# Performance work log

Hardware: AMD Instinct MI355X
Metric: run time of the kernel (lower is better)

Reference implementation:

```python
import jax, jax.numpy as jnp
import numpy as np
from jax import lax

B, N, T, HOR, HID = 512, 128, 128, 32, 512


def _uni(k, shape, s):
    return jax.random.uniform(k, shape, jnp.float32, -s, s)


def setup_inputs() -> dict:
    key = jax.random.key(0)
    ks = jax.random.split(key, 24)
    s = 1.0 / np.sqrt(HID)
    inp = {"window": jax.random.normal(ks[0], (B * N, T), jnp.float32)}
    # encoder LSTM (2 layers, torch gate order i,f,g,o)
    inp["Wih0"] = _uni(ks[1], (4 * HID, N), s); inp["Whh0"] = _uni(ks[2], (4 * HID, HID), s)
    inp["bih0"] = _uni(ks[3], (4 * HID,), s);   inp["bhh0"] = _uni(ks[4], (4 * HID,), s)
    inp["Wih1"] = _uni(ks[5], (4 * HID, HID), s); inp["Whh1"] = _uni(ks[6], (4 * HID, HID), s)
    inp["bih1"] = _uni(ks[7], (4 * HID,), s);     inp["bhh1"] = _uni(ks[8], (4 * HID,), s)
    # decoder cells
    inp["Wc1i"] = _uni(ks[9], (4 * HID, N), s);   inp["Wc1h"] = _uni(ks[10], (4 * HID, HID), s)
    inp["bc1i"] = _uni(ks[11], (4 * HID,), s);    inp["bc1h"] = _uni(ks[12], (4 * HID,), s)
    inp["Wc2i"] = _uni(ks[13], (4 * HID, HID), s); inp["Wc2h"] = _uni(ks[14], (4 * HID, HID), s)
    inp["bc2i"] = _uni(ks[15], (4 * HID,), s);     inp["bc2h"] = _uni(ks[16], (4 * HID,), s)
    # output projection
    inp["Wp"] = _uni(ks[17], (N, HID), s); inp["bp"] = _uni(ks[18], (N,), s)
    # deterministic inverted-dropout masks
    keep_e = 0.75  # nn.LSTM inter-layer dropout p=0.25
    keep_d = 0.8   # F.dropout p=0.2 in decode loop
    inp["enc_mask"] = (jax.random.uniform(ks[19], (T, B, HID)) < keep_e).astype(jnp.float32) / keep_e
    inp["dec_h_mask"] = (jax.random.uniform(ks[20], (HOR - 1, B, HID)) < keep_d).astype(jnp.float32) / keep_d
    inp["dec_c_mask"] = (jax.random.uniform(ks[21], (HOR - 1, B, HID)) < keep_d).astype(jnp.float32) / keep_d
    return inp


def _cell(x, h, c, Wih, Whh, bih, bhh):
    g = x @ Wih.T + h @ Whh.T + (bih + bhh)
    i, f, gg, o = jnp.split(g, 4, axis=-1)
    c = jax.nn.sigmoid(f) * c + jax.nn.sigmoid(i) * jnp.tanh(gg)
    h = jax.nn.sigmoid(o) * jnp.tanh(c)
    return h, c


def _run_layer(xs, Wih, Whh, bih, bhh):
    # xs: [T, B, D] -> outputs [T, B, HID], final (h, c)
    h0 = jnp.zeros((xs.shape[1], HID), xs.dtype)
    def step(carry, x):
        h, c = carry
        h, c = _cell(x, h, c, Wih, Whh, bih, bhh)
        return (h, c), h
    (h, c), hs = lax.scan(step, (h0, h0), xs)
    return hs, h, c


def reference(window, Wih0, Whh0, bih0, bhh0, Wih1, Whh1, bih1, bhh1,
              Wc1i, Wc1h, bc1i, bc1h, Wc2i, Wc2h, bc2i, bc2h, Wp, bp,
              enc_mask, dec_h_mask, dec_c_mask):
    x = window.reshape(B, T, N).transpose(1, 0, 2)  # [T, B, N]
    hs0, h1, c1 = _run_layer(x, Wih0, Whh0, bih0, bhh0)
    hs0 = hs0 * enc_mask  # inter-layer dropout (training mode)
    _, h2, c2 = _run_layer(hs0, Wih1, Whh1, bih1, bhh1)

    def dec_step(carry, masks):
        h1, c1, h2, c2 = carry
        mh, mc = masks
        pred = h2 @ Wp.T + bp                       # [B, N]
        h1, c1 = _cell(pred, h1, c1, Wc1i, Wc1h, bc1i, bc1h)
        h1 = h1 * mh
        c1 = c1 * mc
        h2, c2 = _cell(h1, h2, c2, Wc2i, Wc2h, bc2i, bc2h)
        return (h1, c1, h2, c2), pred

    (h1, c1, h2, c2), preds = lax.scan(dec_step, (h1, c1, h2, c2), (dec_h_mask, dec_c_mask))
    final = h2 @ Wp.T + bp                          # [B, N]
    allp = jnp.concatenate([preds, final[None]], axis=0)  # [HOR, B, N]
    # torch: each pred.view(-1,1), cat dim=1 -> [B*N, HOR]
    return allp.transpose(1, 2, 0).reshape(B * N, HOR)
```

## Files before the change

### kernel.cpp

```cpp
#include <hip/hip_runtime.h>
#include <math.h>

#define HID 512
#define BAT 512
#define NIN 128
#define TST 128
#define HOR 32
#define SBZ ((size_t)BAT * HID)
#define SL 262144
#define SLB 524288

using bf16x8 = __attribute__((ext_vector_type(8))) __bf16;
using f32x4  = __attribute__((ext_vector_type(4))) float;

__device__ __forceinline__ float sigf(float x) { return 1.0f / (1.0f + __expf(-x)); }
__device__ __forceinline__ float tanhfast(float x) { return 1.0f - 2.0f / (__expf(2.0f * x) + 1.0f); }

__device__ __forceinline__ short f2bf(float x) {
    union { float f; unsigned u; } v; v.f = x;
    unsigned r = (v.u + 0x7FFFu + ((v.u >> 16) & 1u)) >> 16;
    return (short)r;
}
__device__ __forceinline__ float bf2f(short s) {
    union { unsigned u; float f; } v; v.u = ((unsigned)(unsigned short)s) << 16;
    return v.f;
}
__device__ __forceinline__ bf16x8 asbf(f32x4 v) {
    union { f32x4 f; bf16x8 b; } u; u.f = v; return u.b;
}

__device__ __forceinline__ void gbar3(unsigned* bar, int bid, unsigned ep) {
    __syncthreads();
    if (threadIdx.x == 0) {
        unsigned* leaf = bar + ((unsigned)bid >> 3) * 32;
        unsigned* root = bar + 1024;
        unsigned* flag = bar + 1056;
        unsigned old = __hip_atomic_fetch_add(leaf, 1u, __ATOMIC_RELAXED, __HIP_MEMORY_SCOPE_AGENT);
        if (old == 8u * ep - 1u) {
            unsigned ro = __hip_atomic_fetch_add(root, 1u, __ATOMIC_RELAXED, __HIP_MEMORY_SCOPE_AGENT);
            if (ro == 32u * ep - 1u)
                __hip_atomic_store(flag, ep, __ATOMIC_RELAXED, __HIP_MEMORY_SCOPE_AGENT);
        }
        int spin = 0;
        while (__hip_atomic_load(flag, __ATOMIC_RELAXED, __HIP_MEMORY_SCOPE_AGENT) < ep) {
            __builtin_amdgcn_s_sleep(1);
            if (((++spin) & 63) == 0)
                __hip_atomic_fetch_add(flag, 0u, __ATOMIC_RELAXED, __HIP_MEMORY_SCOPE_AGENT);
        }
    }
    __syncthreads();
}


__global__ __launch_bounds__(256) void prep_w(const float* __restrict__ Wih,
                                              const float* __restrict__ Whh,
                                              short* __restrict__ W2, int Kx, int Kp) {
    size_t i = (size_t)blockIdx.x * 256 + threadIdx.x;
    if (i >= (size_t)2048 * Kp) return;
    int np = (int)(i / Kp), kp = (int)(i % Kp);
    int u = np >> 2, gate = np & 3;
    int on = gate * HID + u;
    float w = (kp < Kx) ? Wih[(size_t)on * Kx + kp] : Whh[(size_t)on * HID + (kp - Kx)];
    W2[i] = f2bf(w);
}

__global__ __launch_bounds__(256) void prep_x(const float* __restrict__ window,
                                              short* __restrict__ X2t) {
    size_t i = (size_t)blockIdx.x * 256 + threadIdx.x;
    if (i >= (size_t)TST * BAT * NIN) return;
    int n = (int)(i & 127);
    int b = (int)((i >> 7) & 511);
    int t = (int)(i >> 16);
    float x = window[(size_t)b * (TST * NIN) + (size_t)t * NIN + n];
    int rg = b >> 4;
    int l = (b & 15) + (((n >> 3) & 3) << 4);
    int e = n & 7;
    size_t base = (size_t)t * 65536 + ((size_t)(rg * 4 + (n >> 5)) << 9) + l * 8 + e;
    X2t[base] = f2bf(x);
}

__global__ __launch_bounds__(256) void prep_fuse(const float* __restrict__ Wc1i,
                                                 const float* __restrict__ Wp,
                                                 float* __restrict__ Wfuse) {
    size_t i = (size_t)blockIdx.x * 256 + threadIdx.x;
    if (i >= (size_t)2048 * 512) return;
    int on = (int)(i >> 9), k = (int)(i & 511);
    float s = 0.f;
    for (int n = 0; n < NIN; ++n) s += Wc1i[(size_t)on * NIN + n] * Wp[(size_t)n * HID + k];
    Wfuse[i] = s;
}

__global__ __launch_bounds__(256) void prep_badd(const float* __restrict__ Wc1i,
                                                 const float* __restrict__ bp,
                                                 float* __restrict__ badd) {
    int on = blockIdx.x * 256 + threadIdx.x;
    if (on >= 2048) return;
    float s = 0.f;
    for (int n = 0; n < NIN; ++n) s += Wc1i[(size_t)on * NIN + n] * bp[n];
    badd[on] = s;
}

__global__ __launch_bounds__(256) void prep_bias(const float* __restrict__ bih,
                                                 const float* __restrict__ bhh,
                                                 const float* __restrict__ badd,
                                                 float* __restrict__ bout) {
    int np = blockIdx.x * 256 + threadIdx.x;
    if (np >= 2048) return;
    int on = (np & 3) * HID + (np >> 2);
    float v = bih[on] + bhh[on];
    if (badd) v += badd[on];
    bout[np] = v;
}

__global__ __launch_bounds__(256) void prep_wp(const float* __restrict__ Wp,
                                               short* __restrict__ W2p) {
    int i = blockIdx.x * 256 + threadIdx.x;
    if (i >= 128 * 512) return;
    W2p[i] = f2bf(Wp[i]);
}


__device__ __forceinline__ void gl16sc(f32x4& q, const char* p) {
    asm volatile("global_load_dwordx4 %0, %1, off sc0 sc1" : "=v"(q) : "v"(p));
}

__device__ __forceinline__ void load_wres32(char* lds, const short* Wg, int K) {
    const int tid = threadIdx.x;
    const int r = tid >> 4;
    const int cnt = K >> 7;
    const int jb = (tid & 15) * cnt;
    for (int q = 0; q < cnt; ++q) {
        int j = jb + q;
        bf16x8 v = *(const bf16x8*)(Wg + (size_t)r * K + j * 8);
        *(bf16x8*)(lds + j * 512 + r * 16) = v;
    }
}

__device__ __forceinline__ void load_wres64(char* lds, const short* Wg, int K) {
    const int r = threadIdx.x >> 2, jg = threadIdx.x & 3;
    for (int q = 0; q < (K >> 5); ++q) {
        int j = jg + (q << 2);
        bf16x8 v = *(const bf16x8*)(Wg + (size_t)r * K + j * 8);
        *(bf16x8*)(lds + (size_t)j * 1024 + r * 16) = v;
    }
}

__device__ __forceinline__ void pre_mask_asm(const float* msk, int mrow, int u0, float o[4]) {
    const int lane = threadIdx.x & 63;
    const float* p = msk + (size_t)(mrow + ((lane >> 3) << 2)) * HID + u0 + (lane & 7);
#pragma unroll
    for (int r = 0; r < 4; ++r)
        asm volatile("global_load_dword %0, %1, off" : "=v"(o[r]) : "v"(p + (size_t)r * HID));
}

template<int C0, int C1>
__device__ __forceinline__ void gemm64(
    const char* wres, const short* a0t, const short* a1t,
    int mb, f32x4 acc[2][4])
{
    constexpr int NKC = C0 + C1;
    constexpr int D = 16;
    const int lane = threadIdx.x & 63;
    const int arow = lane & 15, akg = lane >> 4;
    const size_t lb = (size_t)lane << 4;
    const char* base0 = (const char*)a0t;
    const char* base1 = (const char*)a1t;
    auto cptr = [&](int kc, int fh) -> const char* {
        return (kc < C0)
            ? base0 + (((size_t)(mb * 2 + fh) * C0 + kc) << 10) + lb
            : base1 + (((size_t)(mb * 2 + fh) * C1 + (kc - C0)) << 10) + lb;
    };
    f32x4 q0[D], q1[D];
#pragma unroll
    for (int i = 0; i < D; ++i) {
        gl16sc(q0[i], cptr(i, 0));
        gl16sc(q1[i], cptr(i, 1));
    }
#pragma unroll
    for (int kc = 0; kc < NKC; ++kc) {
        const int sl = kc % D;
        asm volatile("s_waitcnt vmcnt(%2)"
                     : "+v"(q0[sl]), "+v"(q1[sl])
                     : "i"((2 * ((NKC - kc) < D ? (NKC - kc) : D)) - 2));
        const bf16x8 fa0 = asbf(q0[sl]);
        const bf16x8 fa1 = asbf(q1[sl]);
        if (kc + D < NKC) {
            gl16sc(q0[sl], cptr(kc + D, 0));
            gl16sc(q1[sl], cptr(kc + D, 1));
        }
        const char* wrow = wres + (size_t)((kc << 2) + akg) * 1024;
        bf16x8 fb[4];
#pragma unroll
        for (int nj = 0; nj < 4; ++nj)
            fb[nj] = *(const bf16x8*)(wrow + ((nj * 16 + arow) << 4));
#pragma unroll
        for (int nj = 0; nj < 4; ++nj) {
            acc[0][nj] = __builtin_amdgcn_mfma_f32_16x16x32_bf16(fa0, fb[nj], acc[0][nj], 0, 0, 0);
            acc[1][nj] = __builtin_amdgcn_mfma_f32_16x16x32_bf16(fa1, fb[nj], acc[1][nj], 0, 0, 0);
        }
    }
    asm volatile("s_waitcnt vmcnt(0)");
}

__device__ __forceinline__ void cell_epi64(
    char* scrw, f32x4 acc[2][4], float creg[2][4], int mb, int np0,
    const float* bias_p, const float* mh, const float* mc, const float* ma,
    short* h_out, short* h_aux)
{
    const int lane = threadIdx.x & 63;
#pragma unroll
    for (int p = 0; p < 2; ++p) {
        const int np0p = np0 + (p << 5);
#pragma unroll
        for (int mi = 0; mi < 2; ++mi)
#pragma unroll
            for (int nj = 0; nj < 2; ++nj) {
                const int row = mi * 16 + ((lane >> 4) << 2);
                const int col = nj * 16 + (lane & 15);
#pragma unroll
                for (int r = 0; r < 4; ++r)
                    *(float*)(scrw + (row + r) * 128 + (col << 2)) = acc[mi][p * 2 + nj][r];
            }
        asm volatile("s_waitcnt lgkmcnt(0)" ::: "memory");
        const int ul = lane & 7, g = lane >> 3;
        f32x4 gv[4];
#pragma unroll
        for (int r = 0; r < 4; ++r)
            gv[r] = *(const f32x4*)(scrw + ((g << 2) + r) * 128 + (ul << 4));
        asm volatile("s_waitcnt lgkmcnt(0)" ::: "memory");
        const float4 bs = *(const float4*)(bias_p + np0p + (ul << 2));
#pragma unroll
        for (int r = 0; r < 4; ++r) {
            const int m = (g << 2) + r;
            const int fh = m >> 4, r16 = m & 15;
            const float gi = gv[r][0] + bs.x, gf = gv[r][1] + bs.y;
            const float gg = gv[r][2] + bs.z, go = gv[r][3] + bs.w;
            const float cn = sigf(gf) * creg[p][r] + sigf(gi) * tanhfast(gg);
            const float h  = sigf(go) * tanhfast(cn);
            creg[p][r] = mc ? cn * mc[p * 4 + r] : cn;
            const float hm = mh ? h * mh[p * 4 + r] : h;
            const int idx2 = (r16 << 3) + ul;
            *(short*)(scrw + fh * 256 + idx2 * 2) = f2bf(hm);
            if (h_aux)
                *(short*)(scrw + 512 + fh * 256 + idx2 * 2) = f2bf(h * ma[p * 4 + r]);
        }
        const int u0p = np0p >> 2;
        const int c_hi = u0p >> 5, gsub = (u0p >> 3) & 3;
        unsigned vmain[2], vaux[2];
#pragma unroll
        for (int s = 0; s < 2; ++s)
            vmain[s] = *(const unsigned*)(scrw + s * 256 + (lane << 2));
        if (h_aux)
#pragma unroll
            for (int s = 0; s < 2; ++s)
                vaux[s] = *(const unsigned*)(scrw + 512 + s * 256 + (lane << 2));
        asm volatile("s_waitcnt lgkmcnt(0)" ::: "memory");
#pragma unroll
        for (int s = 0; s < 2; ++s) {
            const unsigned* dst = (const unsigned*)(h_out
                + ((size_t)((mb * 2 + s) * 16 + c_hi) << 9) + (gsub << 7)) + lane;
            asm volatile("global_store_dword %0, %1, off sc0 sc1" :: "v"(dst), "v"(vmain[s]));
        }
        if (h_aux)
#pragma unroll
            for (int s = 0; s < 2; ++s) {
                const unsigned* dst = (const unsigned*)(h_aux
                    + ((size_t)((mb * 2 + s) * 16 + c_hi) << 9) + (gsub << 7)) + lane;
                asm volatile("global_store_dword %0, %1, off sc0 sc1" :: "v"(dst), "v"(vaux[s]));
            }
    }
}


__global__ void __launch_bounds__(256, 1) persist_kernel(
    const short* __restrict__ X2t,
    const short* __restrict__ W0, const short* __restrict__ W1,
    const short* __restrict__ Wd1, const short* __restrict__ Wd2,
    short* hA0, short* hA1, short* hd0, short* hd1, short* hB0, short* hB1,
    short* hBall0, short* hBallR,
    const float* __restrict__ bias0, const float* __restrict__ bias1,
    const float* __restrict__ biasd1, const float* __restrict__ biasd2,
    const float* __restrict__ enc_mask, const float* __restrict__ dec_h_mask,
    const float* __restrict__ dec_c_mask, unsigned* bar)
{
    extern __shared__ __align__(16) char lds[];
    const int bid = blockIdx.x;
    const int xcd = bid & 7;
    const int half = xcd >> 2;
    const int m0 = (xcd & 3) * 128;
    const int ntile = bid >> 3;
    const int np0 = ntile * 64;
    const int u0 = np0 >> 2;
    const int w = threadIdx.x >> 6;
    const int mb = (m0 >> 5) + w;
    const int mrow = m0 + (w << 5);
    char* scrw = lds + 131072 + (w << 12);
    float creg[2][4] = {{0.f,0.f,0.f,0.f},{0.f,0.f,0.f,0.f}};

    auto hA_rd = [&](int t) -> const short* { return (t & 1) ? hA1 : hA0; };
    auto hA_wr = [&](int t) -> short* { return (t & 1) ? hA0 : hA1; };
    auto hd_at = [&](int t) -> short* { return (t & 1) ? hd1 : hd0; };
    auto hB_rd = [&](int t) -> const short* { return (t & 1) ? hB1 : hB0; };
    auto hB_wr = [&](int t) -> short* { return (t & 1) ? hB0 : hB1; };
    auto decA_at = [&](int i) -> short* { return (i & 1) ? hA1 : hA0; };
    auto hball = [&](int i) -> short* { return (i == 0) ? hBall0 : hBallR + (size_t)(i - 1) * SL; };

    load_wres64(lds, (half ? W1 : W0) + (size_t)np0 * (half ? 1024 : 640), half ? 1024 : 640);
    __syncthreads();
    unsigned ep = 0;
    for (int tt = 0; tt <= TST; ++tt) {
        if (half == 0) {
            if (tt < TST) {
                const int t = tt;
                float ma[8];
                pre_mask_asm(enc_mask + (size_t)t * SBZ, mrow, u0, ma);
                pre_mask_asm(enc_mask + (size_t)t * SBZ, mrow, u0 + 8, ma + 4);
                f32x4 acc[2][4];
#pragma unroll
                for (int a = 0; a < 2; ++a)
#pragma unroll
                    for (int b2 = 0; b2 < 4; ++b2) acc[a][b2] = (f32x4){0.f, 0.f, 0.f, 0.f};
                gemm64<4, 16>(lds, X2t + (size_t)t * 65536, hA_rd(t), mb, acc);
                cell_epi64(scrw, acc, creg, mb, np0, bias0, nullptr, nullptr, ma,
                           hA_wr(t), hd_at(t));
            }
        } else {
            if (tt >= 1) {
                const int t = tt - 1;
                f32x4 acc[2][4];
#pragma unroll
                for (int a = 0; a < 2; ++a)
#pragma unroll
                    for (int b2 = 0; b2 < 4; ++b2) acc[a][b2] = (f32x4){0.f, 0.f, 0.f, 0.f};
                gemm64<16, 16>(lds, hd_at(t), hB_rd(t), mb, acc);
                short* outp = (t == TST - 1) ? hBall0 : hB_wr(t);
                cell_epi64(scrw, acc, creg, mb, np0, bias1, nullptr, nullptr, nullptr,
                           outp, nullptr);
            }
        }
        gbar3(bar, bid, ++ep);
    }

    load_wres64(lds, (half ? Wd2 : Wd1) + (size_t)np0 * 1024, 1024);
    __syncthreads();
    for (int s = 0; s < HOR - 1; ++s) {
        if (half == 0) {
            float mh[8], mc[8];
            pre_mask_asm(dec_h_mask + (size_t)s * SBZ, mrow, u0, mh);
            pre_mask_asm(dec_h_mask + (size_t)s * SBZ, mrow, u0 + 8, mh + 4);
            pre_mask_asm(dec_c_mask + (size_t)s * SBZ, mrow, u0, mc);
            pre_mask_asm(dec_c_mask + (size_t)s * SBZ, mrow, u0 + 8, mc + 4);
            f32x4 acc[2][4];
#pragma unroll
            for (int a = 0; a < 2; ++a)
#pragma unroll
                for (int b2 = 0; b2 < 4; ++b2) acc[a][b2] = (f32x4){0.f, 0.f, 0.f, 0.f};
            gemm64<16, 16>(lds, hball(s), decA_at(s), mb, acc);
            cell_epi64(scrw, acc, creg, mb, np0, biasd1, mh, mc, nullptr,
                       decA_at(s + 1), nullptr);
        }
        gbar3(bar, bid, ++ep);
        if (half == 1) {
            f32x4 acc[2][4];
#pragma unroll
            for (int a = 0; a < 2; ++a)
#pragma unroll
                for (int b2 = 0; b2 < 4; ++b2) acc[a][b2] = (f32x4){0.f, 0.f, 0.f, 0.f};
            gemm64<16, 16>(lds, decA_at(s + 1), hball(s), mb, acc);
            cell_epi64(scrw, acc, creg, mb, np0, biasd2, nullptr, nullptr, nullptr,
                       hball(s + 1), nullptr);
        }
        gbar3(bar, bid, ++ep);
    }
}


template<int C0, int C1>
__device__ __forceinline__ void gemm_pipeP(
    const char* wres, const short* a0t, const short* a1t,
    int mb, f32x4 acc[2][2])
{
    constexpr int NKC = C0 + C1;
    constexpr int D = 16;
    const int lane = threadIdx.x & 63;
    const int arow = lane & 15, akg = lane >> 4;
    const size_t lb = (size_t)lane << 4;
    const char* base0 = (const char*)a0t;
    const char* base1 = (const char*)a1t;
    auto cptr = [&](int kc, int fh) -> const char* {
        return (kc < C0)
            ? base0 + (((size_t)(mb * 2 + fh) * C0 + kc) << 10) + lb
            : base1 + (((size_t)(mb * 2 + fh) * C1 + (kc - C0)) << 10) + lb;
    };
    f32x4 q0[D], q1[D];
#pragma unroll
    for (int i = 0; i < D; ++i) {
        gl16sc(q0[i], cptr(i, 0));
        gl16sc(q1[i], cptr(i, 1));
    }
#pragma unroll
    for (int kc = 0; kc < NKC; ++kc) {
        const int sl = kc % D;
        asm volatile("s_waitcnt vmcnt(%2)"
                     : "+v"(q0[sl]), "+v"(q1[sl])
                     : "i"((2 * ((NKC - kc) < D ? (NKC - kc) : D)) - 2));
        const bf16x8 fa0 = asbf(q0[sl]);
        const bf16x8 fa1 = asbf(q1[sl]);
        if (kc + D < NKC) {
            gl16sc(q0[sl], cptr(kc + D, 0));
            gl16sc(q1[sl], cptr(kc + D, 1));
        }
        const char* wrow = wres + (size_t)(((kc << 2) + akg) << 9);
        const bf16x8 fb0 = *(const bf16x8*)(wrow + (arow << 4));
        const bf16x8 fb1 = *(const bf16x8*)(wrow + ((16 + arow) << 4));
        acc[0][0] = __builtin_amdgcn_mfma_f32_16x16x32_bf16(fa0, fb0, acc[0][0], 0, 0, 0);
        acc[0][1] = __builtin_amdgcn_mfma_f32_16x16x32_bf16(fa0, fb1, acc[0][1], 0, 0, 0);
        acc[1][0] = __builtin_amdgcn_mfma_f32_16x16x32_bf16(fa1, fb0, acc[1][0], 0, 0, 0);
        acc[1][1] = __builtin_amdgcn_mfma_f32_16x16x32_bf16(fa1, fb1, acc[1][1], 0, 0, 0);
    }
    asm volatile("s_waitcnt vmcnt(0)");
}

__global__ void __launch_bounds__(512, 2) proj_kernel(
    const short* hBall0, const short* hBallR, const short* __restrict__ W2p,
    const float* __restrict__ bp, float* __restrict__ pred_all)
{
    extern __shared__ __align__(16) char lds[];
    const int bid = blockIdx.x;
    const int s = bid >> 3, q = bid & 7;
    const int bh = q >> 2, n0p = (q & 3) * 32;
    load_wres32(lds, W2p + (size_t)n0p * 512, 512);
    const int w = threadIdx.x >> 6, lane = threadIdx.x & 63;
    char* scrw = lds + 32768 + w * 4608;
    const int mb = bh * 8 + w;
    const short* A = (s == 0) ? hBall0 : hBallR + (size_t)(s - 1) * SL;
    __syncthreads();
    f32x4 acc[2][2];
#pragma unroll
    for (int a = 0; a < 2; ++a)
#pragma unroll
        for (int b2 = 0; b2 < 2; ++b2) acc[a][b2] = (f32x4){0.f, 0.f, 0.f, 0.f};
    gemm_pipeP<16, 0>(lds, A, A, mb, acc);
#pragma unroll
    for (int mi = 0; mi < 2; ++mi)
#pragma unroll
        for (int ni = 0; ni < 2; ++ni) {
            const int row = mi * 16 + ((lane >> 4) << 2);
            const int col = ni * 16 + (lane & 15);
#pragma unroll
            for (int r = 0; r < 4; ++r)
                *(float*)(scrw + (row + r) * 144 + (col << 2)) = acc[mi][ni][r];
        }
    asm volatile("s_waitcnt lgkmcnt(0)" ::: "memory");
    const int rr = lane >> 1, hf = lane & 1;
    float* dst = pred_all + (size_t)s * (BAT * NIN)
               + (size_t)(bh * 256 + w * 32 + rr) * NIN + n0p + hf * 16;
#pragma unroll
    for (int t4 = 0; t4 < 4; ++t4) {
        f32x4 v = *(const f32x4*)(scrw + rr * 144 + hf * 64 + t4 * 16);
        const float4 b4 = *(const float4*)(bp + n0p + hf * 16 + t4 * 4);
        v[0] += b4.x; v[1] += b4.y; v[2] += b4.z; v[3] += b4.w;
        *(f32x4*)(dst + t4 * 4) = v;
    }
}

__global__ __launch_bounds__(256) void transpose_out(const float* __restrict__ pred_all,
                                                     float* __restrict__ out) {
    __shared__ float tl[32][65];
    const int base = blockIdx.x * 64;
    const int tid = threadIdx.x;
    for (int i = tid; i < 32 * 64; i += 256) {
        int s = i >> 6, f = i & 63;
        tl[s][f] = pred_all[(size_t)s * (BAT * NIN) + base + f];
    }
    __syncthreads();
    for (int i = tid; i < 64 * 32; i += 256) {
        int f = i >> 5, s = i & 31;
        out[(size_t)(base + f) * HOR + s] = tl[s][f];
    }
}


extern "C" void kernel_launch(void* const* d_in, const int* in_sizes, int n_in,
                              void* d_out, int out_size, void* d_ws, size_t ws_size,
                              hipStream_t stream) {
    (void)in_sizes; (void)n_in; (void)out_size; (void)ws_size;
    const float* window = (const float*)d_in[0];
    const float* Wih0 = (const float*)d_in[1];
    const float* Whh0 = (const float*)d_in[2];
    const float* bih0 = (const float*)d_in[3];
    const float* bhh0 = (const float*)d_in[4];
    const float* Wih1 = (const float*)d_in[5];
    const float* Whh1 = (const float*)d_in[6];
    const float* bih1 = (const float*)d_in[7];
    const float* bhh1 = (const float*)d_in[8];
    const float* Wc1i = (const float*)d_in[9];
    const float* Wc1h = (const float*)d_in[10];
    const float* bc1i = (const float*)d_in[11];
    const float* bc1h = (const float*)d_in[12];
    const float* Wc2i = (const float*)d_in[13];
    const float* Wc2h = (const float*)d_in[14];
    const float* bc2i = (const float*)d_in[15];
    const float* bc2h = (const float*)d_in[16];
    const float* Wp   = (const float*)d_in[17];
    const float* bp   = (const float*)d_in[18];
    const float* enc_mask   = (const float*)d_in[19];
    const float* dec_h_mask = (const float*)d_in[20];
    const float* dec_c_mask = (const float*)d_in[21];
    float* out = (float*)d_out;

    char* base = (char*)d_ws;
    size_t off = 0;
    auto take = [&](size_t bytes) -> char* {
        off = (off + 255) & ~(size_t)255;
        char* r = base + off; off += bytes; return r;
    };
    short* W2e0 = (short*)take((size_t)2048 * 640 * 2);
    short* W2e1 = (short*)take((size_t)2048 * 1024 * 2);
    short* W2d1 = (short*)take((size_t)2048 * 1024 * 2);
    short* W2d2 = (short*)take((size_t)2048 * 1024 * 2);
    short* W2p  = (short*)take((size_t)128 * 512 * 2);
    float* Wfuse = (float*)take((size_t)2048 * 512 * 4);
    float* badd  = (float*)take((size_t)2048 * 4);
    float* bias0 = (float*)take((size_t)2048 * 4);
    float* bias1 = (float*)take((size_t)2048 * 4);
    float* biasd1 = (float*)take((size_t)2048 * 4);
    float* biasd2 = (float*)take((size_t)2048 * 4);
    short* hBall0 = (short*)take(SLB);
    float* pred_all = (float*)take((size_t)HOR * BAT * NIN * 4);
    unsigned* bars = (unsigned*)take(16384);
    short* X2t = (short*)take((size_t)TST * 65536 * 2);
    short* hA0 = (short*)take(SLB);
    short* hA1 = (short*)take(SLB);
    short* hd0 = (short*)take(SLB);
    short* hd1 = (short*)take(SLB);
    short* hB0 = (short*)take(SLB);
    short* hB1 = (short*)take(SLB);
    short* hBallR = X2t;

    prep_fuse<<<(2048 * 512 + 255) / 256, 256, 0, stream>>>(Wc1i, Wp, Wfuse);
    prep_badd<<<8, 256, 0, stream>>>(Wc1i, bp, badd);
    prep_wp<<<(128 * 512 + 255) / 256, 256, 0, stream>>>(Wp, W2p);
    prep_w<<<(2048 * 640 + 255) / 256, 256, 0, stream>>>(Wih0, Whh0, W2e0, NIN, 640);
    prep_w<<<(2048 * 1024 + 255) / 256, 256, 0, stream>>>(Wih1, Whh1, W2e1, HID, 1024);
    prep_w<<<(2048 * 1024 + 255) / 256, 256, 0, stream>>>(Wfuse, Wc1h, W2d1, HID, 1024);
    prep_w<<<(2048 * 1024 + 255) / 256, 256, 0, stream>>>(Wc2i, Wc2h, W2d2, HID, 1024);
    prep_bias<<<8, 256, 0, stream>>>(bih0, bhh0, nullptr, bias0);
    prep_bias<<<8, 256, 0, stream>>>(bih1, bhh1, nullptr, bias1);
    prep_bias<<<8, 256, 0, stream>>>(bc1i, bc1h, badd, biasd1);
    prep_bias<<<8, 256, 0, stream>>>(bc2i, bc2h, nullptr, biasd2);
    prep_x<<<(int)(((size_t)TST * BAT * NIN + 255) / 256), 256, 0, stream>>>(window, X2t);
    hipMemsetAsync(hA0, 0, SLB, stream);
    hipMemsetAsync(hB0, 0, SLB, stream);
    hipMemsetAsync(bars, 0, 16384, stream);

    hipFuncSetAttribute((const void*)&persist_kernel,
                        hipFuncAttributeMaxDynamicSharedMemorySize, 163840);
    persist_kernel<<<256, 256, 147456, stream>>>(
        X2t, W2e0, W2e1, W2d1, W2d2,
        hA0, hA1, hd0, hd1, hB0, hB1,
        hBall0, hBallR,
        bias0, bias1, biasd1, biasd2,
        enc_mask, dec_h_mask, dec_c_mask, bars);

    hipFuncSetAttribute((const void*)&proj_kernel,
                        hipFuncAttributeMaxDynamicSharedMemorySize, 69632);
    proj_kernel<<<256, 512, 69632, stream>>>(hBall0, hBallR, W2p, bp, pred_all);

    transpose_out<<<(BAT * NIN) / 64, 256, 0, stream>>>(pred_all, out);
}
```

Baseline: 1.788 ms.

## Replace grid-wide barriers with per-batch-tile partial barriers and relax cache bypass

Each group of 64 blocks that shares a batch tile (mtile) now synchronises only with itself through a separate hierarchical barrier, instead of all 256 blocks using one grid barrier per step. A single grid barrier remains at the encoder/decoder boundary. Loads of read-only data (the X input slice, and activations in the projection kernel) drop the sc0/sc1 cache-bypass bits so they can hit in cache. The intent is lower barrier latency and cheaper loads, relying on the fact that each M tile's recurrence depends only on its own batch rows.

Measured after the change: 1.736 ms. 1.03x faster.

```diff
diff --git a/kernel.cpp b/kernel.cpp
--- a/kernel.cpp
+++ b/kernel.cpp
@@ -27,6 +27,28 @@
 }
 __device__ __forceinline__ bf16x8 asbf(f32x4 v) {
     union { f32x4 f; bf16x8 b; } u; u.f = v; return u.b;
+}
+
+__device__ __forceinline__ void pbar(unsigned* b, int sub, unsigned ep) {
+    __syncthreads();
+    if (threadIdx.x == 0) {
+        unsigned* leaf = b + (sub >> 3) * 32;
+        unsigned* root = b + 512;
+        unsigned* flag = b + 544;
+        unsigned old = __hip_atomic_fetch_add(leaf, 1u, __ATOMIC_RELAXED, __HIP_MEMORY_SCOPE_AGENT);
+        if (old == 8u * ep - 1u) {
+            unsigned ro = __hip_atomic_fetch_add(root, 1u, __ATOMIC_RELAXED, __HIP_MEMORY_SCOPE_AGENT);
+            if (ro == 8u * ep - 1u)
+                __hip_atomic_store(flag, ep, __ATOMIC_RELAXED, __HIP_MEMORY_SCOPE_AGENT);
+        }
+        int spin = 0;
+        while (__hip_atomic_load(flag, __ATOMIC_RELAXED, __HIP_MEMORY_SCOPE_AGENT) < ep) {
+            __builtin_amdgcn_s_sleep(1);
+            if (((++spin) & 63) == 0)
+                __hip_atomic_fetch_add(flag, 0u, __ATOMIC_RELAXED, __HIP_MEMORY_SCOPE_AGENT);
+        }
+    }
+    __syncthreads();
 }
 
 __device__ __forceinline__ void gbar3(unsigned* bar, int bid, unsigned ep) {
@@ -120,8 +142,12 @@
 }
 
 
-__device__ __forceinline__ void gl16sc(f32x4& q, const char* p) {
-    asm volatile("global_load_dwordx4 %0, %1, off sc0 sc1" : "=v"(q) : "v"(p));
+template<bool SC>
+__device__ __forceinline__ void gl16(f32x4& q, const char* p) {
+    if constexpr (SC)
+        asm volatile("global_load_dwordx4 %0, %1, off sc0 sc1" : "=v"(q) : "v"(p));
+    else
+        asm volatile("global_load_dwordx4 %0, %1, off" : "=v"(q) : "v"(p));
 }
 
 __device__ __forceinline__ void load_wres32(char* lds, const short* Wg, int K) {
@@ -153,7 +179,7 @@
         asm volatile("global_load_dword %0, %1, off" : "=v"(o[r]) : "v"(p + (size_t)r * HID));
 }
 
-template<int C0, int C1>
+template<int C0, int C1, bool SC0, bool SC1>
 __device__ __forceinline__ void gemm64(
     const char* wres, const short* a0t, const short* a1t,
     int mb, f32x4 acc[2][4])
@@ -173,8 +199,8 @@
     f32x4 q0[D], q1[D];
 #pragma unroll
     for (int i = 0; i < D; ++i) {
-        gl16sc(q0[i], cptr(i, 0));
-        gl16sc(q1[i], cptr(i, 1));
+        if (i < C0) { gl16<SC0>(q0[i], cptr(i, 0)); gl16<SC0>(q1[i], cptr(i, 1)); }
+        else        { gl16<SC1>(q0[i], cptr(i, 0)); gl16<SC1>(q1[i], cptr(i, 1)); }
     }
 #pragma unroll
     for (int kc = 0; kc < NKC; ++kc) {
@@ -185,8 +211,8 @@
         const bf16x8 fa0 = asbf(q0[sl]);
         const bf16x8 fa1 = asbf(q1[sl]);
         if (kc + D < NKC) {
-            gl16sc(q0[sl], cptr(kc + D, 0));
-            gl16sc(q1[sl], cptr(kc + D, 1));
+            if (kc + D < C0) { gl16<SC0>(q0[sl], cptr(kc + D, 0)); gl16<SC0>(q1[sl], cptr(kc + D, 1)); }
+            else             { gl16<SC1>(q0[sl], cptr(kc + D, 0)); gl16<SC1>(q1[sl], cptr(kc + D, 1)); }
         }
         const char* wrow = wres + (size_t)((kc << 2) + akg) * 1024;
         bf16x8 fb[4];
@@ -287,7 +313,8 @@
     const int bid = blockIdx.x;
     const int xcd = bid & 7;
     const int half = xcd >> 2;
-    const int m0 = (xcd & 3) * 128;
+    const int mtile = xcd & 3;
+    const int m0 = mtile * 128;
     const int ntile = bid >> 3;
     const int np0 = ntile * 64;
     const int u0 = np0 >> 2;
@@ -296,6 +323,10 @@
     const int mrow = m0 + (w << 5);
     char* scrw = lds + 131072 + (w << 12);
     float creg[2][4] = {{0.f,0.f,0.f,0.f},{0.f,0.f,0.f,0.f}};
+
+    unsigned* pb = bar + mtile * 1024;
+    unsigned* gb = bar + 4096;
+    const int sub = (half << 5) | ntile;
 
     auto hA_rd = [&](int t) -> const short* { return (t & 1) ? hA1 : hA0; };
     auto hA_wr = [&](int t) -> short* { return (t & 1) ? hA0 : hA1; };
@@ -320,7 +351,7 @@
                 for (int a = 0; a < 2; ++a)
 #pragma unroll
                     for (int b2 = 0; b2 < 4; ++b2) acc[a][b2] = (f32x4){0.f, 0.f, 0.f, 0.f};
-                gemm64<4, 16>(lds, X2t + (size_t)t * 65536, hA_rd(t), mb, acc);
+                gemm64<4, 16, false, true>(lds, X2t + (size_t)t * 65536, hA_rd(t), mb, acc);
                 cell_epi64(scrw, acc, creg, mb, np0, bias0, nullptr, nullptr, ma,
                            hA_wr(t), hd_at(t));
             }
@@ -332,14 +363,16 @@
                 for (int a = 0; a < 2; ++a)
 #pragma unroll
                     for (int b2 = 0; b2 < 4; ++b2) acc[a][b2] = (f32x4){0.f, 0.f, 0.f, 0.f};
-                gemm64<16, 16>(lds, hd_at(t), hB_rd(t), mb, acc);
+                gemm64<16, 16, true, true>(lds, hd_at(t), hB_rd(t), mb, acc);
                 short* outp = (t == TST - 1) ? hBall0 : hB_wr(t);
                 cell_epi64(scrw, acc, creg, mb, np0, bias1, nullptr, nullptr, nullptr,
                            outp, nullptr);
             }
         }
-        gbar3(bar, bid, ++ep);
-    }
+        pbar(pb, sub, ++ep);
+    }
+
+    gbar3(gb, bid, 1u);
 
     load_wres64(lds, (half ? Wd2 : Wd1) + (size_t)np0 * 1024, 1024);
     __syncthreads();
@@ -355,22 +388,22 @@
             for (int a = 0; a < 2; ++a)
 #pragma unroll
                 for (int b2 = 0; b2 < 4; ++b2) acc[a][b2] = (f32x4){0.f, 0.f, 0.f, 0.f};
-            gemm64<16, 16>(lds, hball(s), decA_at(s), mb, acc);
+            gemm64<16, 16, true, true>(lds, hball(s), decA_at(s), mb, acc);
             cell_epi64(scrw, acc, creg, mb, np0, biasd1, mh, mc, nullptr,
                        decA_at(s + 1), nullptr);
         }
-        gbar3(bar, bid, ++ep);
+        pbar(pb, sub, ++ep);
         if (half == 1) {
             f32x4 acc[2][4];
 #pragma unroll
             for (int a = 0; a < 2; ++a)
 #pragma unroll
                 for (int b2 = 0; b2 < 4; ++b2) acc[a][b2] = (f32x4){0.f, 0.f, 0.f, 0.f};
-            gemm64<16, 16>(lds, decA_at(s + 1), hball(s), mb, acc);
+            gemm64<16, 16, true, true>(lds, decA_at(s + 1), hball(s), mb, acc);
             cell_epi64(scrw, acc, creg, mb, np0, biasd2, nullptr, nullptr, nullptr,
                        hball(s + 1), nullptr);
         }
-        gbar3(bar, bid, ++ep);
+        pbar(pb, sub, ++ep);
     }
 }
 
@@ -395,8 +428,8 @@
     f32x4 q0[D], q1[D];
 #pragma unroll
     for (int i = 0; i < D; ++i) {
-        gl16sc(q0[i], cptr(i, 0));
-        gl16sc(q1[i], cptr(i, 1));
+        gl16<false>(q0[i], cptr(i, 0));
+        gl16<false>(q1[i], cptr(i, 1));
     }
 #pragma unroll
     for (int kc = 0; kc < NKC; ++kc) {
@@ -407,8 +440,8 @@
         const bf16x8 fa0 = asbf(q0[sl]);
         const bf16x8 fa1 = asbf(q1[sl]);
         if (kc + D < NKC) {
-            gl16sc(q0[sl], cptr(kc + D, 0));
-            gl16sc(q1[sl], cptr(kc + D, 1));
+            gl16<false>(q0[sl], cptr(kc + D, 0));
+            gl16<false>(q1[sl], cptr(kc + D, 1));
         }
         const char* wrow = wres + (size_t)(((kc << 2) + akg) << 9);
         const bf16x8 fb0 = *(const bf16x8*)(wrow + (arow << 4));
@@ -528,7 +561,7 @@
     float* biasd2 = (float*)take((size_t)2048 * 4);
     short* hBall0 = (short*)take(SLB);
     float* pred_all = (float*)take((size_t)HOR * BAT * NIN * 4);
-    unsigned* bars = (unsigned*)take(16384);
+    unsigned* bars = (unsigned*)take(32768);
     short* X2t = (short*)take((size_t)TST * 65536 * 2);
     short* hA0 = (short*)take(SLB);
     short* hA1 = (short*)take(SLB);
@@ -552,7 +585,7 @@
     prep_x<<<(int)(((size_t)TST * BAT * NIN + 255) / 256), 256, 0, stream>>>(window, X2t);
     hipMemsetAsync(hA0, 0, SLB, stream);
     hipMemsetAsync(hB0, 0, SLB, stream);
-    hipMemsetAsync(bars, 0, 16384, stream);
+    hipMemsetAsync(bars, 0, 32768, stream);
 
     hipFuncSetAttribute((const void*)&persist_kernel,
                         hipFuncAttributeMaxDynamicSharedMemorySize, 163840);
```
